# Performance work log

Measured on AMD Instinct MI355X. Metric: run time of the kernel, lower is better.

The kernel has to match this reference:

```python
import jax, jax.numpy as jnp
import numpy as np
import math

B = 524288
D = 4
CTX = 64
HID = 128
IN_DIM = 2 + CTX  # keep_idx len is 2 for every mask
# default_masks_D(4, 10) dedups to exactly these 4 masks (torch module therefore has 4 layers)
KEEP = ((0, 1), (1, 2), (2, 3), (0, 3))
TRANS = ((2, 3), (0, 3), (0, 1), (1, 2))
L = 4


def _mlp(x, W1, b1, W2, b2, W3, b3):
    # MLP(in_dim, out_dim, hidden=128, depth=2): Lin+GELU, Lin+GELU, Lin
    x = jax.nn.gelu(x @ W1 + b1, approximate=False)
    x = jax.nn.gelu(x @ W2 + b2, approximate=False)
    return x @ W3 + b3


def setup_inputs() -> dict:
    key = jax.random.key(0)
    ks = jax.random.split(key, 16)
    theta = jax.random.normal(ks[0], (B, D), dtype=jnp.float32)
    h = jax.random.normal(ks[1], (B, CTX), dtype=jnp.float32)
    p = lambda k, shape: jax.random.normal(k, shape, dtype=jnp.float32) * 0.02
    inp = {"theta": theta, "h": h}
    # stacked per-layer weights for s_net and t_net
    for pref, off in (("s", 2), ("t", 8)):
        inp[pref + "W1"] = p(ks[off + 0], (L, IN_DIM, HID))
        inp[pref + "b1"] = p(ks[off + 1], (L, HID))
        inp[pref + "W2"] = p(ks[off + 2], (L, HID, HID))
        inp[pref + "b2"] = p(ks[off + 3], (L, HID))
        inp[pref + "W3"] = p(ks[off + 4], (L, HID, 2))
        inp[pref + "b3"] = p(ks[off + 5], (L, 2))
    return inp


def reference(theta, h, sW1, sb1, sW2, sb2, sW3, sb3, tW1, tb1, tW2, tb2, tW3, tb3):
    # ConditionalRealNVP.log_prob(theta, h)
    x = theta
    logdet = jnp.zeros(theta.shape[0], dtype=theta.dtype)
    for i in range(L):
        keep = np.array(KEEP[i])
        trans = np.array(TRANS[i])
        xp = jnp.concatenate([x[:, keep], h], axis=1)  # [B, 66]
        s = _mlp(xp, sW1[i], sb1[i], sW2[i], sb2[i], sW3[i], sb3[i])  # [B, 2]
        t = _mlp(xp, tW1[i], tb1[i], tW2[i], tb2[i], tW3[i], tb3[i])  # [B, 2]
        x = x.at[:, trans].set(x[:, trans] * jnp.exp(s) + t)
        logdet = logdet + s.sum(axis=1)
    log_pz = -0.5 * (x ** 2).sum(axis=1) - 0.5 * D * math.log(2 * math.pi)
    return log_pz + logdet
```

## Files before the change

### kernel.cpp

```cpp
#include <hip/hip_runtime.h>
#include <hip/hip_bf16.h>

typedef short short8 __attribute__((ext_vector_type(8)));
typedef float f32x4 __attribute__((ext_vector_type(4)));
typedef unsigned short u16;
typedef u16 u16x8 __attribute__((ext_vector_type(8)));

#define NL_STRIDE 57344
#define OFF_W1F 0
#define OFF_W2F 16384
#define OFF_W3F 49152
#define OFF_W1K 53248
#define OFF_B1  54272
#define OFF_B2  54784
#define OFF_B3  55296

__device__ __forceinline__ u16 f2bf(float f) {
  union { float f; unsigned int u; } v; v.f = f;
  unsigned int r = v.u + 0x7fffu + ((v.u >> 16) & 1u);
  return (u16)(r >> 16);
}

__device__ __forceinline__ float gelu_fast(float x) {
  float u = x * x;
  float t = fmaf(0.00417617f, u, -0.0560330f);
  t = fmaf(t, u, 0.394326f);
  float s = fmaf(x, t, 0.5f);
  s = __builtin_amdgcn_fmed3f(s, 0.0f, 1.0f);
  return x * s;
}

__global__ __launch_bounds__(256) void prep_kernel(
    const float* __restrict__ sW1, const float* __restrict__ sb1,
    const float* __restrict__ sW2, const float* __restrict__ sb2,
    const float* __restrict__ sW3, const float* __restrict__ sb3,
    const float* __restrict__ tW1, const float* __restrict__ tb1,
    const float* __restrict__ tW2, const float* __restrict__ tb2,
    const float* __restrict__ tW3, const float* __restrict__ tb3,
    char* __restrict__ ws)
{
  int nl = blockIdx.x;
  int layer = nl >> 1, net = nl & 1;
  const float* W1 = net ? tW1 : sW1;
  const float* W2 = net ? tW2 : sW2;
  const float* W3 = net ? tW3 : sW3;
  const float* B1 = net ? tb1 : sb1;
  const float* B2 = net ? tb2 : sb2;
  const float* B3 = net ? tb3 : sb3;
  char* base = ws + (size_t)nl * NL_STRIDE;
  int e = blockIdx.y * 256 + (int)threadIdx.x;

  if (e < 8192) {
    int kt = e >> 12, rem = e & 4095, nt = rem >> 9, r2 = rem & 511;
    int l = r2 >> 3, j = r2 & 7;
    int k = kt * 32 + (l >> 4) * 8 + j, n = nt * 16 + (l & 15);
    ((u16*)(base + OFF_W1F))[e] = f2bf(W1[layer * 8448 + (2 + k) * 128 + n]);
  } else if (e < 24576) {
    int e2 = e - 8192;
    int kt = e2 >> 12, nt = (e2 >> 9) & 7, l = (e2 >> 3) & 63, j = e2 & 7;
    int k = kt * 32 + (l >> 4) * 8 + j, n = nt * 16 + (l & 15);
    ((u16*)(base + OFF_W2F))[e2] = f2bf(W2[layer * 16384 + k * 128 + n]);
  } else if (e < 26624) {
    int e3 = e - 24576;
    int kt = e3 >> 9, l = (e3 >> 3) & 63, j = e3 & 7;
    int k = kt * 32 + (l >> 4) * 8 + j, n = l & 15;
    float v = (n < 2) ? W3[layer * 256 + k * 2 + n] : 0.0f;
    ((u16*)(base + OFF_W3F))[e3] = f2bf(v);
  } else if (e < 26880) {
    int e4 = e - 26624; int r = e4 >> 7, n = e4 & 127;
    ((float*)(base + OFF_W1K))[e4] = W1[layer * 8448 + r * 128 + n];
  } else if (e < 27008) {
    int e5 = e - 26880; ((float*)(base + OFF_B1))[e5] = B1[layer * 128 + e5];
  } else if (e < 27136) {
    int e6 = e - 27008; ((float*)(base + OFF_B2))[e6] = B2[layer * 128 + e6];
  } else if (e < 27138) {
    int e7 = e - 27136; ((float*)(base + OFF_B3))[e7] = B3[layer * 2 + e7];
  }
}

__global__ __launch_bounds__(256, 2) void realnvp_kernel(
    const float* __restrict__ theta, const float* __restrict__ h_g,
    const char* __restrict__ ws, float* __restrict__ out)
{
  __shared__ __align__(16) u16 hs[128 * 72];
  __shared__ __align__(16) u16 hid[128 * 136];
  __shared__ float x_lds[128 * 4];
  __shared__ float sbuf[2 * 128 * 2];

  const int tid = (int)threadIdx.x;
  const int row0 = (int)blockIdx.x * 128;
  const int wv = tid >> 6, lane = tid & 63, q = lane >> 4, lr = lane & 15;

  if (tid < 128) {
    float4 t4 = *(const float4*)(theta + (size_t)(row0 + tid) * 4);
    x_lds[tid * 4 + 0] = t4.x; x_lds[tid * 4 + 1] = t4.y;
    x_lds[tid * 4 + 2] = t4.z; x_lds[tid * 4 + 3] = t4.w;
  }
  {
    int r = tid >> 1, hf = tid & 1;
    const float* src = h_g + (size_t)(row0 + r) * 64 + hf * 32;
    u16* dst = &hs[r * 72 + hf * 32];
#pragma unroll
    for (int c = 0; c < 32; c += 8) {
      float4 f0 = *(const float4*)(src + c);
      float4 f1 = *(const float4*)(src + c + 4);
      u16x8 o;
      o[0] = f2bf(f0.x); o[1] = f2bf(f0.y); o[2] = f2bf(f0.z); o[3] = f2bf(f0.w);
      o[4] = f2bf(f1.x); o[5] = f2bf(f1.y); o[6] = f2bf(f1.z); o[7] = f2bf(f1.w);
      *(u16x8*)(dst + c) = o;
    }
  }
  __syncthreads();

  float logdet = 0.0f;
  const f32x4 zero4 = {0.f, 0.f, 0.f, 0.f};
  const int col0 = wv * 32 + lr;

#pragma unroll 1
  for (int layer = 0; layer < 4; ++layer) {
    int k0 = (0x0210 >> (layer * 4)) & 15;
    int k1 = (0x3321 >> (layer * 4)) & 15;

#pragma unroll 1
    for (int net = 0; net < 2; ++net) {
      const char* base = ws + (size_t)(layer * 2 + net) * NL_STRIDE;
      const u16* w1f = (const u16*)(base + OFF_W1F);
      const u16* w2f = (const u16*)(base + OFF_W2F);
      const u16* w3f = (const u16*)(base + OFF_W3F);
      const float* w1k = (const float*)(base + OFF_W1K);
      const float* b1 = (const float*)(base + OFF_B1);
      const float* b2 = (const float*)(base + OFF_B2);
      const float* b3 = (const float*)(base + OFF_B3);

      f32x4 acc[8][2];
#pragma unroll
      for (int mt = 0; mt < 8; ++mt) { acc[mt][0] = zero4; acc[mt][1] = zero4; }
      {
        const u16* abase = &hs[lr * 72 + q * 8];
#pragma unroll
        for (int kt = 0; kt < 2; ++kt) {
          short8 a[8];
#pragma unroll
          for (int mt = 0; mt < 8; ++mt)
            a[mt] = *(const short8*)(abase + mt * (16 * 72) + kt * 32);
          short8 b0 = *(const short8*)(w1f + (kt * 8 + wv * 2 + 0) * 512 + lane * 8);
          short8 b1v = *(const short8*)(w1f + (kt * 8 + wv * 2 + 1) * 512 + lane * 8);
#pragma unroll
          for (int mt = 0; mt < 8; ++mt) {
            acc[mt][0] = __builtin_amdgcn_mfma_f32_16x16x32_bf16(a[mt], b0, acc[mt][0], 0, 0, 0);
            acc[mt][1] = __builtin_amdgcn_mfma_f32_16x16x32_bf16(a[mt], b1v, acc[mt][1], 0, 0, 0);
          }
        }
      }
      float wk00 = w1k[col0],       wk01 = w1k[col0 + 16];
      float wk10 = w1k[128 + col0], wk11 = w1k[128 + col0 + 16];
      float bb0 = b1[col0], bb1 = b1[col0 + 16];
      __syncthreads();
#pragma unroll
      for (int mt = 0; mt < 8; ++mt) {
        int rb = mt * 16 + q * 4;
#pragma unroll
        for (int r = 0; r < 4; ++r) {
          int row = rb + r;
          float xk0 = x_lds[row * 4 + k0], xk1 = x_lds[row * 4 + k1];
          float v0 = acc[mt][0][r] + xk0 * wk00 + xk1 * wk10 + bb0;
          float v1 = acc[mt][1][r] + xk0 * wk01 + xk1 * wk11 + bb1;
          hid[row * 136 + col0]      = f2bf(gelu_fast(v0));
          hid[row * 136 + col0 + 16] = f2bf(gelu_fast(v1));
        }
      }
      __syncthreads();

      f32x4 acc2[8][2];
#pragma unroll
      for (int mt = 0; mt < 8; ++mt) { acc2[mt][0] = zero4; acc2[mt][1] = zero4; }
      {
        const u16* hbase = &hid[lr * 136 + q * 8];
#pragma unroll
        for (int kt = 0; kt < 4; ++kt) {
          short8 a[8];
#pragma unroll
          for (int mt = 0; mt < 8; ++mt)
            a[mt] = *(const short8*)(hbase + mt * (16 * 136) + kt * 32);
          short8 b0 = *(const short8*)(w2f + (kt * 8 + wv * 2 + 0) * 512 + lane * 8);
          short8 b1v = *(const short8*)(w2f + (kt * 8 + wv * 2 + 1) * 512 + lane * 8);
#pragma unroll
          for (int mt = 0; mt < 8; ++mt) {
            acc2[mt][0] = __builtin_amdgcn_mfma_f32_16x16x32_bf16(a[mt], b0, acc2[mt][0], 0, 0, 0);
            acc2[mt][1] = __builtin_amdgcn_mfma_f32_16x16x32_bf16(a[mt], b1v, acc2[mt][1], 0, 0, 0);
          }
        }
      }
      float cb0 = b2[col0], cb1 = b2[col0 + 16];
      __syncthreads();
#pragma unroll
      for (int mt = 0; mt < 8; ++mt) {
        int rb = mt * 16 + q * 4;
#pragma unroll
        for (int r = 0; r < 4; ++r) {
          int row = rb + r;
          hid[row * 136 + col0]      = f2bf(gelu_fast(acc2[mt][0][r] + cb0));
          hid[row * 136 + col0 + 16] = f2bf(gelu_fast(acc2[mt][1][r] + cb1));
        }
      }
      __syncthreads();

      f32x4 acc3[2]; acc3[0] = zero4; acc3[1] = zero4;
#pragma unroll
      for (int kt = 0; kt < 4; ++kt) {
        short8 b = *(const short8*)(w3f + kt * 512 + lane * 8);
#pragma unroll
        for (int i = 0; i < 2; ++i) {
          short8 a = *(const short8*)(&hid[((wv * 2 + i) * 16 + lr) * 136 + kt * 32 + q * 8]);
          acc3[i] = __builtin_amdgcn_mfma_f32_16x16x32_bf16(a, b, acc3[i], 0, 0, 0);
        }
      }
      if (lr < 2) {
        float bb = b3[lr];
#pragma unroll
        for (int i = 0; i < 2; ++i) {
          int rb = (wv * 2 + i) * 16 + q * 4;
#pragma unroll
          for (int r = 0; r < 4; ++r)
            sbuf[net * 256 + (rb + r) * 2 + lr] = acc3[i][r] + bb;
        }
      }
      __syncthreads();
    }

    if (tid < 128) {
      float s0 = sbuf[tid * 2 + 0], s1 = sbuf[tid * 2 + 1];
      float t0 = sbuf[256 + tid * 2 + 0], t1 = sbuf[256 + tid * 2 + 1];
      int a0 = (0x1002 >> (layer * 4)) & 15;
      int a1 = (0x2133 >> (layer * 4)) & 15;
      x_lds[tid * 4 + a0] = x_lds[tid * 4 + a0] * __expf(s0) + t0;
      x_lds[tid * 4 + a1] = x_lds[tid * 4 + a1] * __expf(s1) + t1;
      logdet += s0 + s1;
    }
    __syncthreads();
  }

  if (tid < 128) {
    float x0 = x_lds[tid * 4 + 0], x1 = x_lds[tid * 4 + 1];
    float x2 = x_lds[tid * 4 + 2], x3 = x_lds[tid * 4 + 3];
    out[row0 + tid] = -0.5f * (x0 * x0 + x1 * x1 + x2 * x2 + x3 * x3)
                      - 3.6757541328f + logdet;
  }
}

extern "C" void kernel_launch(void* const* d_in, const int* in_sizes, int n_in,
                              void* d_out, int out_size, void* d_ws, size_t ws_size,
                              hipStream_t stream) {
  (void)in_sizes; (void)n_in; (void)out_size; (void)ws_size;
  const float* theta = (const float*)d_in[0];
  const float* h     = (const float*)d_in[1];
  const float* sW1 = (const float*)d_in[2],  *sb1 = (const float*)d_in[3];
  const float* sW2 = (const float*)d_in[4],  *sb2 = (const float*)d_in[5];
  const float* sW3 = (const float*)d_in[6],  *sb3 = (const float*)d_in[7];
  const float* tW1 = (const float*)d_in[8],  *tb1 = (const float*)d_in[9];
  const float* tW2 = (const float*)d_in[10], *tb2 = (const float*)d_in[11];
  const float* tW3 = (const float*)d_in[12], *tb3 = (const float*)d_in[13];
  float* out = (float*)d_out;
  char* ws = (char*)d_ws;

  dim3 pgrid(8, 107);
  prep_kernel<<<pgrid, 256, 0, stream>>>(sW1, sb1, sW2, sb2, sW3, sb3,
                                         tW1, tb1, tW2, tb2, tW3, tb3, ws);
  realnvp_kernel<<<4096, 256, 0, stream>>>(theta, h, (const char*)ws, out);
}
```

Before: 615.6 us.

## Pack paired hidden outputs into 32-bit LDS stores with permuted K and packed math

Each lane's two hidden columns (col0 and col0+16) are now written as one packed 32-bit bf16 pair. The W2/W3 K ordering is permuted in the prep kernel so the GEMM still reads the correct weights from that interleaved layout. GELU and the bias/FMA epilogue use float2 vectors so the compiler can emit packed FP32 instructions. Bf16 conversion switches to cheaper round-half-up packing, which changes rounding slightly; the goal is fewer LDS store instructions and less ALU work in the epilogues.

Result: slower. 638.6 us (+3.7%).

```diff
diff --git a/kernel.cpp b/kernel.cpp
--- a/kernel.cpp
+++ b/kernel.cpp
@@ -3,8 +3,10 @@
 
 typedef short short8 __attribute__((ext_vector_type(8)));
 typedef float f32x4 __attribute__((ext_vector_type(4)));
+typedef float f32x2 __attribute__((ext_vector_type(2)));
 typedef unsigned short u16;
-typedef u16 u16x8 __attribute__((ext_vector_type(8)));
+typedef unsigned int u32;
+typedef u32 u32x4 __attribute__((ext_vector_type(4)));
 
 #define NL_STRIDE 57344
 #define OFF_W1F 0
@@ -21,13 +23,25 @@
   return (u16)(r >> 16);
 }
 
-__device__ __forceinline__ float gelu_fast(float x) {
-  float u = x * x;
-  float t = fmaf(0.00417617f, u, -0.0560330f);
-  t = fmaf(t, u, 0.394326f);
-  float s = fmaf(x, t, 0.5f);
-  s = __builtin_amdgcn_fmed3f(s, 0.0f, 1.0f);
+__device__ __forceinline__ u32 pack_bf16_2(float a, float b) {
+  union { float f; u32 u; } x, y; x.f = a; y.f = b;
+  u32 ra = x.u + 0x8000u, rb = y.u + 0x8000u;
+  return (ra >> 16) | (rb & 0xffff0000u);
+}
+
+__device__ __forceinline__ f32x2 gelu2(f32x2 x) {
+  f32x2 u = x * x;
+  f32x2 t = u * 0.00417617f + (-0.0560330f);
+  t = t * u + 0.394326f;
+  f32x2 s = x * t + 0.5f;
+  s.x = __builtin_amdgcn_fmed3f(s.x, 0.0f, 1.0f);
+  s.y = __builtin_amdgcn_fmed3f(s.y, 0.0f, 1.0f);
   return x * s;
+}
+
+__device__ __forceinline__ int kperm(int k) {
+  int b = k & 31;
+  return (k & ~31) | ((b >> 1) | ((b & 1) << 4));
 }
 
 __global__ __launch_bounds__(256) void prep_kernel(
@@ -59,12 +73,12 @@
     int e2 = e - 8192;
     int kt = e2 >> 12, nt = (e2 >> 9) & 7, l = (e2 >> 3) & 63, j = e2 & 7;
     int k = kt * 32 + (l >> 4) * 8 + j, n = nt * 16 + (l & 15);
-    ((u16*)(base + OFF_W2F))[e2] = f2bf(W2[layer * 16384 + k * 128 + n]);
+    ((u16*)(base + OFF_W2F))[e2] = f2bf(W2[layer * 16384 + kperm(k) * 128 + n]);
   } else if (e < 26624) {
     int e3 = e - 24576;
     int kt = e3 >> 9, l = (e3 >> 3) & 63, j = e3 & 7;
     int k = kt * 32 + (l >> 4) * 8 + j, n = l & 15;
-    float v = (n < 2) ? W3[layer * 256 + k * 2 + n] : 0.0f;
+    float v = (n < 2) ? W3[layer * 256 + kperm(k) * 2 + n] : 0.0f;
     ((u16*)(base + OFF_W3F))[e3] = f2bf(v);
   } else if (e < 26880) {
     int e4 = e - 26624; int r = e4 >> 7, n = e4 & 127;
@@ -104,10 +118,12 @@
     for (int c = 0; c < 32; c += 8) {
       float4 f0 = *(const float4*)(src + c);
       float4 f1 = *(const float4*)(src + c + 4);
-      u16x8 o;
-      o[0] = f2bf(f0.x); o[1] = f2bf(f0.y); o[2] = f2bf(f0.z); o[3] = f2bf(f0.w);
-      o[4] = f2bf(f1.x); o[5] = f2bf(f1.y); o[6] = f2bf(f1.z); o[7] = f2bf(f1.w);
-      *(u16x8*)(dst + c) = o;
+      u32x4 o;
+      o[0] = pack_bf16_2(f0.x, f0.y);
+      o[1] = pack_bf16_2(f0.z, f0.w);
+      o[2] = pack_bf16_2(f1.x, f1.y);
+      o[3] = pack_bf16_2(f1.z, f1.w);
+      *(u32x4*)(dst + c) = o;
     }
   }
   __syncthreads();
@@ -115,6 +131,7 @@
   float logdet = 0.0f;
   const f32x4 zero4 = {0.f, 0.f, 0.f, 0.f};
   const int col0 = wv * 32 + lr;
+  u32* hidw = (u32*)&hid[wv * 32 + lr * 2];
 
 #pragma unroll 1
   for (int layer = 0; layer < 4; ++layer) {
@@ -152,9 +169,9 @@
           }
         }
       }
-      float wk00 = w1k[col0],       wk01 = w1k[col0 + 16];
-      float wk10 = w1k[128 + col0], wk11 = w1k[128 + col0 + 16];
-      float bb0 = b1[col0], bb1 = b1[col0 + 16];
+      f32x2 wk0 = {w1k[col0],       w1k[col0 + 16]};
+      f32x2 wk1 = {w1k[128 + col0], w1k[128 + col0 + 16]};
+      f32x2 bb  = {b1[col0],        b1[col0 + 16]};
       __syncthreads();
 #pragma unroll
       for (int mt = 0; mt < 8; ++mt) {
@@ -163,10 +180,12 @@
         for (int r = 0; r < 4; ++r) {
           int row = rb + r;
           float xk0 = x_lds[row * 4 + k0], xk1 = x_lds[row * 4 + k1];
-          float v0 = acc[mt][0][r] + xk0 * wk00 + xk1 * wk10 + bb0;
-          float v1 = acc[mt][1][r] + xk0 * wk01 + xk1 * wk11 + bb1;
-          hid[row * 136 + col0]      = f2bf(gelu_fast(v0));
-          hid[row * 136 + col0 + 16] = f2bf(gelu_fast(v1));
+          f32x2 v = {acc[mt][0][r], acc[mt][1][r]};
+          v = wk0 * xk0 + v;
+          v = wk1 * xk1 + v;
+          v = v + bb;
+          f32x2 g = gelu2(v);
+          hidw[row * 68] = pack_bf16_2(g.x, g.y);
         }
       }
       __syncthreads();
@@ -191,7 +210,7 @@
           }
         }
       }
-      float cb0 = b2[col0], cb1 = b2[col0 + 16];
+      f32x2 cb = {b2[col0], b2[col0 + 16]};
       __syncthreads();
 #pragma unroll
       for (int mt = 0; mt < 8; ++mt) {
@@ -199,8 +218,9 @@
 #pragma unroll
         for (int r = 0; r < 4; ++r) {
           int row = rb + r;
-          hid[row * 136 + col0]      = f2bf(gelu_fast(acc2[mt][0][r] + cb0));
-          hid[row * 136 + col0 + 16] = f2bf(gelu_fast(acc2[mt][1][r] + cb1));
+          f32x2 v = {acc2[mt][0][r], acc2[mt][1][r]};
+          f32x2 g = gelu2(v + cb);
+          hidw[row * 68] = pack_bf16_2(g.x, g.y);
         }
       }
       __syncthreads();
@@ -216,13 +236,13 @@
         }
       }
       if (lr < 2) {
-        float bb = b3[lr];
+        float bbs = b3[lr];
 #pragma unroll
         for (int i = 0; i < 2; ++i) {
           int rb = (wv * 2 + i) * 16 + q * 4;
 #pragma unroll
           for (int r = 0; r < 4; ++r)
-            sbuf[net * 256 + (rb + r) * 2 + lr] = acc3[i][r] + bb;
+            sbuf[net * 256 + (rb + r) * 2 + lr] = acc3[i][r] + bbs;
         }
       }
       __syncthreads();
```
